# Kernel tuning notes

Hardware: AMD Instinct MI355X
Metric: run time of the kernel (lower is better)

Reference implementation:

```python
import jax, jax.numpy as jnp
import numpy as np

N, E, G = 50000, 1600000, 64
D_IN, D_EDGE, D_H, D_U, D_OUT = 32, 32, 64, 16, 32


def _linear_params(key, d_in, d_out):
    kw, kb = jax.random.split(key)
    lim = 1.0 / np.sqrt(d_in)
    W = jax.random.uniform(kw, (d_in, d_out), minval=-lim, maxval=lim, dtype=jnp.float32)
    b = jax.random.uniform(kb, (d_out,), minval=-lim, maxval=lim, dtype=jnp.float32)
    return W, b


def setup_inputs() -> dict:
    key = jax.random.key(0)
    ks = jax.random.split(key, 10)
    x = jax.random.normal(ks[0], (N, D_IN), dtype=jnp.float32)
    edge_index = jax.random.randint(ks[1], (2, E), 0, N, dtype=jnp.int64)
    edge_attr = jax.random.normal(ks[2], (E, D_EDGE), dtype=jnp.float32)
    u = jax.random.normal(ks[3], (G, D_U), dtype=jnp.float32)
    batch = jnp.sort(jax.random.randint(ks[4], (N,), 0, G, dtype=jnp.int64))
    W1a, b1a = _linear_params(ks[5], D_IN + D_EDGE, D_H)   # node linear 0
    W1b, b1b = _linear_params(ks[6], D_H, D_H)             # node linear 1 (hidden)
    W2a, b2a = _linear_params(ks[7], D_IN + D_H + D_U, D_H)
    W2b, b2b = _linear_params(ks[8], D_H, D_OUT)
    return dict(x=x, edge_index=edge_index, edge_attr=edge_attr, u=u, batch=batch,
                W1a=W1a, b1a=b1a, W1b=W1b, b1b=b1b,
                W2a=W2a, b2a=b2a, W2b=W2b, b2b=b2b)


def reference(x, edge_index, edge_attr, u, batch,
              W1a, b1a, W1b, b1b, W2a, b2a, W2b, b2b):
    row, col = edge_index[0], edge_index[1]
    # edge-level MLP on [x[col] || edge_attr]
    h = jnp.concatenate([x[col], edge_attr], axis=1)          # [E, D_IN+D_EDGE]
    h = jax.nn.relu(h @ W1a + b1a)                            # [E, D_H]
    h = jax.nn.relu(h @ W1b + b1b)                            # [E, D_H]
    # scatter_mean over destination nodes (row), dim_size = N
    summed = jax.ops.segment_sum(h, row, num_segments=N)      # [N, D_H]
    counts = jax.ops.segment_sum(jnp.ones((h.shape[0],), h.dtype), row, num_segments=N)
    agg = summed / jnp.maximum(counts, 1.0)[:, None]
    # node-level MLP on [x || agg || u[batch]]
    z = jnp.concatenate([x, agg, u[batch]], axis=1)           # [N, D_IN+D_H+D_U]
    z = jax.nn.relu(z @ W2a + b2a)
    return z @ W2b + b2b                                      # [N, D_OUT]
```

## Files before the change

kernel.cpp:

```cpp
#include <hip/hip_runtime.h>
#include <hip/hip_bf16.h>


typedef __attribute__((ext_vector_type(8))) short bf16x8;
typedef __attribute__((ext_vector_type(4))) float f32x4;

__device__ __forceinline__ unsigned short f2bf(float f) {
    __bf16 h = (__bf16)f;
    unsigned short u;
    __builtin_memcpy(&u, &h, 2);
    return u;
}


__global__ __launch_bounds__(256) void count_rows(
    const int* __restrict__ erow, int* __restrict__ counts, int E)
{
    const int gid = blockIdx.x * blockDim.x + threadIdx.x;
    const int stride = gridDim.x * blockDim.x;
    const int n4 = E >> 2;
    for (int i = gid; i < n4; i += stride) {
        const int4 r = ((const int4*)erow)[i];
        atomicAdd(&counts[r.x], 1);
        atomicAdd(&counts[r.y], 1);
        atomicAdd(&counts[r.z], 1);
        atomicAdd(&counts[r.w], 1);
    }
    for (int i = (n4 << 2) + gid; i < E; i += stride)
        atomicAdd(&counts[erow[i]], 1);
}

__global__ __launch_bounds__(256) void scan_blocks(
    const int* __restrict__ counts, int* __restrict__ excl,
    int* __restrict__ bsum, int N)
{
    __shared__ int tmp[256];
    const int t = threadIdx.x;
    const int i = blockIdx.x * 256 + t;
    const int v = (i < N) ? counts[i] : 0;
    tmp[t] = v; __syncthreads();
#pragma unroll
    for (int o = 1; o < 256; o <<= 1) {
        const int a = (t >= o) ? tmp[t - o] : 0;
        __syncthreads();
        tmp[t] += a;
        __syncthreads();
    }
    if (i < N) excl[i] = tmp[t] - v;
    if (t == 255) bsum[blockIdx.x] = tmp[t];
}

__global__ __launch_bounds__(256) void scan_bsum(int* __restrict__ bsum, int nb)
{
    __shared__ int tmp[256];
    const int t = threadIdx.x;
    const int v = (t < nb) ? bsum[t] : 0;
    tmp[t] = v; __syncthreads();
#pragma unroll
    for (int o = 1; o < 256; o <<= 1) {
        const int a = (t >= o) ? tmp[t - o] : 0;
        __syncthreads();
        tmp[t] += a;
        __syncthreads();
    }
    if (t < nb) bsum[t] = tmp[t] - v;
}

__global__ __launch_bounds__(256) void scan_add(
    int* __restrict__ rowstart, int* __restrict__ cursor,
    const int* __restrict__ bsum, int N, int E)
{
    const int i = blockIdx.x * 256 + threadIdx.x;
    if (i < N) {
        const int v = rowstart[i] + bsum[blockIdx.x];
        rowstart[i] = v;
        cursor[i]   = v;
    }
    if (i == 0) rowstart[N] = E;
}

__global__ __launch_bounds__(256) void permute_edges(
    const int* __restrict__ erow, const int* __restrict__ ecol,
    int* __restrict__ cursor, int2* __restrict__ sorted2, int E)
{
    const int gid = blockIdx.x * blockDim.x + threadIdx.x;
    const int stride = gridDim.x * blockDim.x;
    const int n4 = E >> 2;
    for (int i = gid; i < n4; i += stride) {
        const int4 r = ((const int4*)erow)[i];
        const int4 c = ((const int4*)ecol)[i];
        const int e0 = i << 2;
        int pos;
        pos = atomicAdd(&cursor[r.x], 1);
        sorted2[pos] = int2{e0,     (int)((unsigned)c.x | ((unsigned)r.x << 16))};
        pos = atomicAdd(&cursor[r.y], 1);
        sorted2[pos] = int2{e0 + 1, (int)((unsigned)c.y | ((unsigned)r.y << 16))};
        pos = atomicAdd(&cursor[r.z], 1);
        sorted2[pos] = int2{e0 + 2, (int)((unsigned)c.z | ((unsigned)r.z << 16))};
        pos = atomicAdd(&cursor[r.w], 1);
        sorted2[pos] = int2{e0 + 3, (int)((unsigned)c.w | ((unsigned)r.w << 16))};
    }
    for (int i = (n4 << 2) + gid; i < E; i += stride) {
        const int r = erow[i];
        const int pos = atomicAdd(&cursor[r], 1);
        sorted2[pos] = int2{i, (int)((unsigned)ecol[i] | ((unsigned)r << 16))};
    }
}


__global__ __launch_bounds__(256, 3) void edge_mlp_mfma(
    const float* __restrict__ x,
    const int2*  __restrict__ sorted2,
    const float* __restrict__ eattr,
    const float* __restrict__ W1a,
    const float* __restrict__ b1a,
    const float* __restrict__ W1b,
    const float* __restrict__ b1b,
    float* __restrict__ summed,
    int E)
{
    __shared__ __align__(16) unsigned short H2[4 * 16 * 64];

    const int tid  = threadIdx.x;
    const int lane = tid & 63;
    const int wv   = tid >> 6;
    const int g    = lane >> 4;
    const int el   = lane & 15;

    unsigned short* const h2w = H2 + wv * (16 * 64);

    bf16x8 wa[4][2], wb[4][2];
    f32x4  bias1[4];
    float  bias2s[4];
#pragma unroll
    for (int mt = 0; mt < 4; ++mt) {
        const int o = mt * 16 + el;
#pragma unroll
        for (int ks = 0; ks < 2; ++ks) {
            bf16x8 ta, tb;
#pragma unroll
            for (int j = 0; j < 8; ++j) {
                const int k = ks * 32 + 8 * g + j;
                ta[j] = (short)f2bf(W1a[k * 64 + o]);
                tb[j] = (short)f2bf(W1b[k * 64 + o]);
            }
            wa[mt][ks] = ta;
            wb[mt][ks] = tb;
        }
#pragma unroll
        for (int r = 0; r < 4; ++r) bias1[mt][r] = b1a[mt * 16 + 4 * g + r];
        bias2s[mt] = b1b[o];
    }

    const int ntile = (E + 15) >> 4;
    const int wid   = blockIdx.x * 4 + wv;
    const int nw    = gridDim.x * 4;

    const int sw = el & 7;

    for (int t = wid; t < ntile; t += nw) {
        const int ebase = t << 4;

        int2 s2; int row;
        if (ebase + el < E) {
            s2 = sorted2[ebase + el];
            row = (int)((unsigned)s2.y >> 16);
        } else { s2 = int2{0, 0}; row = -1; }

        bf16x8 bf0, bf1;
        {
            const float4* xp = (const float4*)(x + (size_t)(s2.y & 0xFFFF) * 32 + 8 * g);
            const float4* ap = (const float4*)(eattr + (size_t)s2.x * 32 + 8 * g);
            const float4 x0 = xp[0], x1 = xp[1];
            const float4 a0v = ap[0], a1v = ap[1];
            bf0[0] = (short)f2bf(x0.x); bf0[1] = (short)f2bf(x0.y);
            bf0[2] = (short)f2bf(x0.z); bf0[3] = (short)f2bf(x0.w);
            bf0[4] = (short)f2bf(x1.x); bf0[5] = (short)f2bf(x1.y);
            bf0[6] = (short)f2bf(x1.z); bf0[7] = (short)f2bf(x1.w);
            bf1[0] = (short)f2bf(a0v.x); bf1[1] = (short)f2bf(a0v.y);
            bf1[2] = (short)f2bf(a0v.z); bf1[3] = (short)f2bf(a0v.w);
            bf1[4] = (short)f2bf(a1v.x); bf1[5] = (short)f2bf(a1v.y);
            bf1[6] = (short)f2bf(a1v.z); bf1[7] = (short)f2bf(a1v.w);
        }

        f32x4 a0 = bias1[0], a1 = bias1[1], a2 = bias1[2], a3 = bias1[3];
        a0 = __builtin_amdgcn_mfma_f32_16x16x32_bf16(wa[0][0], bf0, a0, 0, 0, 0);
        a1 = __builtin_amdgcn_mfma_f32_16x16x32_bf16(wa[1][0], bf0, a1, 0, 0, 0);
        a2 = __builtin_amdgcn_mfma_f32_16x16x32_bf16(wa[2][0], bf0, a2, 0, 0, 0);
        a3 = __builtin_amdgcn_mfma_f32_16x16x32_bf16(wa[3][0], bf0, a3, 0, 0, 0);
        a0 = __builtin_amdgcn_mfma_f32_16x16x32_bf16(wa[0][1], bf1, a0, 0, 0, 0);
        a1 = __builtin_amdgcn_mfma_f32_16x16x32_bf16(wa[1][1], bf1, a1, 0, 0, 0);
        a2 = __builtin_amdgcn_mfma_f32_16x16x32_bf16(wa[2][1], bf1, a2, 0, 0, 0);
        a3 = __builtin_amdgcn_mfma_f32_16x16x32_bf16(wa[3][1], bf1, a3, 0, 0, 0);

        unsigned short* hrow = h2w + el * 64;
        {
            f32x4 accs[4] = {a0, a1, a2, a3};
#pragma unroll
            for (int mt = 0; mt < 4; ++mt) {
                unsigned short pk[4];
#pragma unroll
                for (int r = 0; r < 4; ++r) pk[r] = f2bf(fmaxf(accs[mt][r], 0.f));
                const int hid   = mt * 16 + 4 * g;
                const int chunk = hid >> 3;
                const int off   = hid & 7;
                *(uint2*)(hrow + ((chunk ^ sw) * 8 + off)) = *(uint2*)pk;
            }
        }

        const bf16x8 hb0 = *(const bf16x8*)(hrow + (((0 + g) ^ sw) * 8));
        const bf16x8 hb1 = *(const bf16x8*)(hrow + (((4 + g) ^ sw) * 8));
        f32x4 d0 = {bias2s[0], bias2s[0], bias2s[0], bias2s[0]};
        f32x4 d1 = {bias2s[1], bias2s[1], bias2s[1], bias2s[1]};
        f32x4 d2 = {bias2s[2], bias2s[2], bias2s[2], bias2s[2]};
        f32x4 d3 = {bias2s[3], bias2s[3], bias2s[3], bias2s[3]};
        d0 = __builtin_amdgcn_mfma_f32_16x16x32_bf16(hb0, wb[0][0], d0, 0, 0, 0);
        d1 = __builtin_amdgcn_mfma_f32_16x16x32_bf16(hb0, wb[1][0], d1, 0, 0, 0);
        d2 = __builtin_amdgcn_mfma_f32_16x16x32_bf16(hb0, wb[2][0], d2, 0, 0, 0);
        d3 = __builtin_amdgcn_mfma_f32_16x16x32_bf16(hb0, wb[3][0], d3, 0, 0, 0);
        d0 = __builtin_amdgcn_mfma_f32_16x16x32_bf16(hb1, wb[0][1], d0, 0, 0, 0);
        d1 = __builtin_amdgcn_mfma_f32_16x16x32_bf16(hb1, wb[1][1], d1, 0, 0, 0);
        d2 = __builtin_amdgcn_mfma_f32_16x16x32_bf16(hb1, wb[2][1], d2, 0, 0, 0);
        d3 = __builtin_amdgcn_mfma_f32_16x16x32_bf16(hb1, wb[3][1], d3, 0, 0, 0);

#pragma unroll
        for (int r = 0; r < 4; ++r) {
            d0[r] = fmaxf(d0[r], 0.f);
            d1[r] = fmaxf(d1[r], 0.f);
            d2[r] = fmaxf(d2[r], 0.f);
            d3[r] = fmaxf(d3[r], 0.f);
        }

        const int prevrow = __shfl(row, lane - 1);
        unsigned long long bmask =
            __ballot((g == 0) && (el > 0) && (row != prevrow));
        bmask = (bmask & 0xFFFEull) | 0x10000ull;

        int s = 0;
        while (s < 16) {
            const int e = s + 1 + (__ffsll(bmask >> (s + 1)) - 1);
            const int rowid = __shfl(row, s);
            if (rowid >= 0) {
                float s0 = 0.f, s1 = 0.f, s2v = 0.f, s3 = 0.f;
#pragma unroll
                for (int r = 0; r < 4; ++r) {
                    const int ej = 4 * g + r;
                    const bool in = (ej >= s) && (ej < e);
                    s0  += in ? d0[r] : 0.f;
                    s1  += in ? d1[r] : 0.f;
                    s2v += in ? d2[r] : 0.f;
                    s3  += in ? d3[r] : 0.f;
                }
                s0  += __shfl_xor(s0, 16);  s0  += __shfl_xor(s0, 32);
                s1  += __shfl_xor(s1, 16);  s1  += __shfl_xor(s1, 32);
                s2v += __shfl_xor(s2v, 16); s2v += __shfl_xor(s2v, 32);
                s3  += __shfl_xor(s3, 16);  s3  += __shfl_xor(s3, 32);
                const float val = (g == 0) ? s0 : (g == 1) ? s1
                                : (g == 2) ? s2v : s3;
                unsafeAtomicAdd(&summed[(size_t)rowid * 64 + lane], val);
            }
            s = e;
        }
    }
}


__global__ __launch_bounds__(256, 2) void node_mlp_mfma(
    const float* __restrict__ x,
    const float* __restrict__ summed,
    const int*   __restrict__ rowstart,
    const float* __restrict__ u,
    const int*   __restrict__ batch,
    const float* __restrict__ W2a,
    const float* __restrict__ b2a,
    const float* __restrict__ W2b,
    const float* __restrict__ b2b,
    float* __restrict__ out,
    int N)
{
    __shared__ __align__(16) unsigned short In[64 * 128];
    __shared__ __align__(16) unsigned short H[64 * 64];

    const int tid  = threadIdx.x;
    const int lane = tid & 63;
    const int wv   = tid >> 6;
    const int g    = lane >> 4;
    const int el   = lane & 15;

    bf16x8 wa[4][4];
    f32x4  bias1[4];
#pragma unroll
    for (int mt = 0; mt < 4; ++mt) {
        const int o = mt * 16 + el;
#pragma unroll
        for (int ks = 0; ks < 4; ++ks) {
            bf16x8 ta;
#pragma unroll
            for (int j = 0; j < 8; ++j) {
                const int k = ks * 32 + 8 * g + j;
                ta[j] = (k < 112) ? (short)f2bf(W2a[k * 64 + o]) : (short)0;
            }
            wa[mt][ks] = ta;
        }
#pragma unroll
        for (int r = 0; r < 4; ++r) bias1[mt][r] = b2a[mt * 16 + 4 * g + r];
    }
    bf16x8 wb[2][2];
    float  bias2s[2];
#pragma unroll
    for (int nt = 0; nt < 2; ++nt) {
        const int o = nt * 16 + el;
#pragma unroll
        for (int ks = 0; ks < 2; ++ks) {
            bf16x8 tb;
#pragma unroll
            for (int j = 0; j < 8; ++j) {
                const int k = ks * 32 + 8 * g + j;
                tb[j] = (short)f2bf(W2b[k * 32 + o]);
            }
            wb[nt][ks] = tb;
        }
        bias2s[nt] = b2b[o];
    }

    unsigned short* const inrow = In + (wv * 16) * 128;
    unsigned short* const hrow0 = H + (wv * 16) * 64;

    const int ntile = (N + 15) >> 4;
    const int wid   = blockIdx.x * 4 + wv;
    const int nw    = gridDim.x * 4;

    for (int t = wid; t < ntile; t += nw) {
        const int nbase = t << 4;

        {
            const int le = lane >> 2;
            const int p  = lane & 3;
            const int n  = nbase + le;
            float4 v[8];
            if (n < N) {
                if (p == 0) {
                    const float4* xp = (const float4*)(x + (size_t)n * 32);
#pragma unroll
                    for (int q = 0; q < 8; ++q) v[q] = xp[q];
                } else if (p < 3) {
                    const int cnt = rowstart[n + 1] - rowstart[n];
                    const float inv = 1.0f / fmaxf((float)cnt, 1.0f);
                    const float4* sp = (const float4*)(summed + (size_t)n * 64 + (p - 1) * 32);
#pragma unroll
                    for (int q = 0; q < 8; ++q) {
                        v[q] = sp[q];
                        v[q].x *= inv; v[q].y *= inv; v[q].z *= inv; v[q].w *= inv;
                    }
                } else {
                    const int gb = batch[n];
                    const float4* up = (const float4*)(u + (size_t)gb * 16);
#pragma unroll
                    for (int q = 0; q < 4; ++q) v[q] = up[q];
#pragma unroll
                    for (int q = 4; q < 8; ++q) v[q] = float4{0.f, 0.f, 0.f, 0.f};
                }
            } else {
#pragma unroll
                for (int q = 0; q < 8; ++q) v[q] = float4{0.f, 0.f, 0.f, 0.f};
            }
            const int sw = le & 7;
            unsigned short* row = inrow + le * 128;
#pragma unroll
            for (int q = 0; q < 4; ++q) {
                bf16x8 c;
                const float4 va = v[2 * q], vb = v[2 * q + 1];
                c[0] = (short)f2bf(va.x); c[1] = (short)f2bf(va.y);
                c[2] = (short)f2bf(va.z); c[3] = (short)f2bf(va.w);
                c[4] = (short)f2bf(vb.x); c[5] = (short)f2bf(vb.y);
                c[6] = (short)f2bf(vb.z); c[7] = (short)f2bf(vb.w);
                const int cc = 4 * p + q;
                const int ci = (cc & 8) | ((cc & 7) ^ sw);
                *(bf16x8*)(row + ci * 8) = c;
            }
        }

        const unsigned short* brow = inrow + el * 128;
        const int sw7 = el & 7;
        f32x4 a0 = bias1[0], a1 = bias1[1], a2 = bias1[2], a3 = bias1[3];
#pragma unroll
        for (int ks = 0; ks < 4; ++ks) {
            const int cc = ks * 4 + g;
            const int ci = (cc & 8) | ((cc & 7) ^ sw7);
            const bf16x8 bf = *(const bf16x8*)(brow + ci * 8);
            a0 = __builtin_amdgcn_mfma_f32_16x16x32_bf16(wa[0][ks], bf, a0, 0, 0, 0);
            a1 = __builtin_amdgcn_mfma_f32_16x16x32_bf16(wa[1][ks], bf, a1, 0, 0, 0);
            a2 = __builtin_amdgcn_mfma_f32_16x16x32_bf16(wa[2][ks], bf, a2, 0, 0, 0);
            a3 = __builtin_amdgcn_mfma_f32_16x16x32_bf16(wa[3][ks], bf, a3, 0, 0, 0);
        }

        unsigned short* hrow = hrow0 + el * 64;
        {
            f32x4 accs[4] = {a0, a1, a2, a3};
#pragma unroll
            for (int mt = 0; mt < 4; ++mt) {
                unsigned short pk[4];
#pragma unroll
                for (int r = 0; r < 4; ++r) pk[r] = f2bf(fmaxf(accs[mt][r], 0.f));
                const int hid   = mt * 16 + 4 * g;
                const int chunk = hid >> 3;
                const int off   = hid & 7;
                *(uint2*)(hrow + ((chunk ^ sw7) * 8 + off)) = *(uint2*)pk;
            }
        }

        const bf16x8 hb0 = *(const bf16x8*)(hrow + (((0 + g) ^ sw7) * 8));
        const bf16x8 hb1 = *(const bf16x8*)(hrow + (((4 + g) ^ sw7) * 8));
        f32x4 dn0 = {bias2s[0], bias2s[0], bias2s[0], bias2s[0]};
        f32x4 dn1 = {bias2s[1], bias2s[1], bias2s[1], bias2s[1]};
        dn0 = __builtin_amdgcn_mfma_f32_16x16x32_bf16(hb0, wb[0][0], dn0, 0, 0, 0);
        dn1 = __builtin_amdgcn_mfma_f32_16x16x32_bf16(hb0, wb[1][0], dn1, 0, 0, 0);
        dn0 = __builtin_amdgcn_mfma_f32_16x16x32_bf16(hb1, wb[0][1], dn0, 0, 0, 0);
        dn1 = __builtin_amdgcn_mfma_f32_16x16x32_bf16(hb1, wb[1][1], dn1, 0, 0, 0);

        if (nbase + 16 <= N) {
#pragma unroll
            for (int r = 0; r < 4; ++r) {
                float* dst = out + (size_t)(nbase + 4 * g + r) * 32 + el;
                dst[0]  = dn0[r];
                dst[16] = dn1[r];
            }
        } else {
#pragma unroll
            for (int r = 0; r < 4; ++r) {
                const int n = nbase + 4 * g + r;
                if (n < N) {
                    float* dst = out + (size_t)n * 32 + el;
                    dst[0]  = dn0[r];
                    dst[16] = dn1[r];
                }
            }
        }
    }
}

extern "C" void kernel_launch(void* const* d_in, const int* in_sizes, int n_in,
                              void* d_out, int out_size, void* d_ws, size_t ws_size,
                              hipStream_t stream) {
    const float* x     = (const float*)d_in[0];
    const int*   eidx  = (const int*)d_in[1];
    const float* eattr = (const float*)d_in[2];
    const float* u     = (const float*)d_in[3];
    const int*   batch = (const int*)d_in[4];
    const float* W1a   = (const float*)d_in[5];
    const float* b1a   = (const float*)d_in[6];
    const float* W1b   = (const float*)d_in[7];
    const float* b1b   = (const float*)d_in[8];
    const float* W2a   = (const float*)d_in[9];
    const float* b2a   = (const float*)d_in[10];
    const float* W2b   = (const float*)d_in[11];
    const float* b2b   = (const float*)d_in[12];
    float* out = (float*)d_out;

    const int N = in_sizes[0] / 32;
    const int E = in_sizes[1] / 2;
    const int* erow = eidx;
    const int* ecol = eidx + E;

    int2*  sorted2  = (int2*)d_ws;
    float* summed   = (float*)(sorted2 + E);
    int*   counts   = (int*)(summed + (size_t)N * 64);
    int*   rowstart = counts + N;
    int*   cursor   = rowstart + (N + 1);
    int*   bsum     = cursor + N;

    hipMemsetAsync(summed, 0, ((size_t)N * 64 + N) * sizeof(float), stream);

    count_rows<<<1024, 256, 0, stream>>>(erow, counts, E);
    const int nb = (N + 255) / 256;
    scan_blocks<<<nb, 256, 0, stream>>>(counts, rowstart, bsum, N);
    scan_bsum<<<1, 256, 0, stream>>>(bsum, nb);
    scan_add<<<nb, 256, 0, stream>>>(rowstart, cursor, bsum, N, E);
    permute_edges<<<1024, 256, 0, stream>>>(erow, ecol, cursor, sorted2, E);

    edge_mlp_mfma<<<4096, 256, 0, stream>>>(x, sorted2, eattr,
                                            W1a, b1a, W1b, b1b, summed, E);
    node_mlp_mfma<<<784, 256, 0, stream>>>(x, summed, rowstart, u, batch,
                                           W2a, b2a, W2b, b2b, out, N);
}
```

Baseline: 314.7 us.

## Pre-convert x and edge_attr to bf16, scattering edge_attr into sorted order

Adds a conversion of x to bf16 inside the row-count kernel. It also replaces the permute kernel with one that writes edge_attr as bf16 directly in row-sorted order, plus packed row/col indices. The edge MLP then reads contiguous bf16 edge features and bf16 x rows instead of gathering fp32 edge_attr by original edge id. This is meant to cut random gather traffic in the edge kernel, at the cost of an extra full pass writing E*64 bytes and needing a larger workspace, with a fallback to the old path when the workspace is too small.

```diff
diff --git a/kernel.cpp b/kernel.cpp
--- a/kernel.cpp
+++ b/kernel.cpp
@@ -11,13 +11,27 @@
     __builtin_memcpy(&u, &h, 2);
     return u;
 }
-
-
-__global__ __launch_bounds__(256) void count_rows(
-    const int* __restrict__ erow, int* __restrict__ counts, int E)
+__device__ __forceinline__ bf16x8 pack8(const float4 a, const float4 b) {
+    bf16x8 c;
+    c[0] = (short)f2bf(a.x); c[1] = (short)f2bf(a.y);
+    c[2] = (short)f2bf(a.z); c[3] = (short)f2bf(a.w);
+    c[4] = (short)f2bf(b.x); c[5] = (short)f2bf(b.y);
+    c[6] = (short)f2bf(b.z); c[7] = (short)f2bf(b.w);
+    return c;
+}
+
+
+__global__ __launch_bounds__(256) void count_rows_convx(
+    const int* __restrict__ erow, int* __restrict__ counts, int E,
+    const float* __restrict__ x, unsigned short* __restrict__ xbf, int nx8)
 {
     const int gid = blockIdx.x * blockDim.x + threadIdx.x;
     const int stride = gridDim.x * blockDim.x;
+    for (int i = gid; i < nx8; i += stride) {
+        const float4 a = ((const float4*)x)[2 * i];
+        const float4 b = ((const float4*)x)[2 * i + 1];
+        *(bf16x8*)(xbf + (size_t)i * 8) = pack8(a, b);
+    }
     const int n4 = E >> 2;
     for (int i = gid; i < n4; i += stride) {
         const int4 r = ((const int4*)erow)[i];
@@ -77,6 +91,27 @@
         cursor[i]   = v;
     }
     if (i == 0) rowstart[N] = E;
+}
+
+__global__ __launch_bounds__(256) void permute_conv(
+    const int* __restrict__ erow, const int* __restrict__ ecol,
+    const float* __restrict__ eattr,
+    int* __restrict__ cursor, int* __restrict__ sorted1,
+    unsigned short* __restrict__ eattr_s, int E)
+{
+    const int gid = blockIdx.x * blockDim.x + threadIdx.x;
+    const int stride = gridDim.x * blockDim.x;
+    for (int i = gid; i < E; i += stride) {
+        const int r = erow[i];
+        const int c = ecol[i];
+        const int pos = atomicAdd(&cursor[r], 1);
+        sorted1[pos] = (int)((unsigned)c | ((unsigned)r << 16));
+        const float4* src = (const float4*)(eattr + (size_t)i * 32);
+        unsigned short* dst = eattr_s + (size_t)pos * 32;
+#pragma unroll
+        for (int q = 0; q < 4; ++q)
+            *(bf16x8*)(dst + 8 * q) = pack8(src[2 * q], src[2 * q + 1]);
+    }
 }
 
 __global__ __launch_bounds__(256) void permute_edges(
@@ -108,16 +143,13 @@
 }
 
 
-__global__ __launch_bounds__(256, 3) void edge_mlp_mfma(
-    const float* __restrict__ x,
-    const int2*  __restrict__ sorted2,
-    const float* __restrict__ eattr,
-    const float* __restrict__ W1a,
-    const float* __restrict__ b1a,
-    const float* __restrict__ W1b,
-    const float* __restrict__ b1b,
-    float* __restrict__ summed,
-    int E)
+__global__ __launch_bounds__(256, 3) void edge_mlp_v2(
+    const unsigned short* __restrict__ xbf,
+    const int*            __restrict__ sorted1,
+    const unsigned short* __restrict__ eattr_s,
+    const float* __restrict__ W1a,  const float* __restrict__ b1a,
+    const float* __restrict__ W1b,  const float* __restrict__ b1b,
+    float* __restrict__ summed, int E)
 {
     __shared__ __align__(16) unsigned short H2[4 * 16 * 64];
 
@@ -155,12 +187,151 @@
     const int ntile = (E + 15) >> 4;
     const int wid   = blockIdx.x * 4 + wv;
     const int nw    = gridDim.x * 4;
-
-    const int sw = el & 7;
+    const int sw    = el & 7;
 
     for (int t = wid; t < ntile; t += nw) {
         const int ebase = t << 4;
-
+        const int e     = ebase + el;
+
+        int row, col;
+        if (e < E) {
+            const int m = sorted1[e];
+            row = (int)((unsigned)m >> 16);
+            col = m & 0xFFFF;
+        } else { row = -1; col = 0; }
+
+        const int ee = (e < E) ? e : (E - 1);
+        const bf16x8 bf0 = *(const bf16x8*)(xbf + (size_t)col * 32 + 8 * g);
+        const bf16x8 bf1 = *(const bf16x8*)(eattr_s + (size_t)ee * 32 + 8 * g);
+
+        f32x4 a0 = bias1[0], a1 = bias1[1], a2 = bias1[2], a3 = bias1[3];
+        a0 = __builtin_amdgcn_mfma_f32_16x16x32_bf16(wa[0][0], bf0, a0, 0, 0, 0);
+        a1 = __builtin_amdgcn_mfma_f32_16x16x32_bf16(wa[1][0], bf0, a1, 0, 0, 0);
+        a2 = __builtin_amdgcn_mfma_f32_16x16x32_bf16(wa[2][0], bf0, a2, 0, 0, 0);
+        a3 = __builtin_amdgcn_mfma_f32_16x16x32_bf16(wa[3][0], bf0, a3, 0, 0, 0);
+        a0 = __builtin_amdgcn_mfma_f32_16x16x32_bf16(wa[0][1], bf1, a0, 0, 0, 0);
+        a1 = __builtin_amdgcn_mfma_f32_16x16x32_bf16(wa[1][1], bf1, a1, 0, 0, 0);
+        a2 = __builtin_amdgcn_mfma_f32_16x16x32_bf16(wa[2][1], bf1, a2, 0, 0, 0);
+        a3 = __builtin_amdgcn_mfma_f32_16x16x32_bf16(wa[3][1], bf1, a3, 0, 0, 0);
+
+        unsigned short* hrow = h2w + el * 64;
+        {
+            f32x4 accs[4] = {a0, a1, a2, a3};
+#pragma unroll
+            for (int mt = 0; mt < 4; ++mt) {
+                unsigned short pk[4];
+#pragma unroll
+                for (int r = 0; r < 4; ++r) pk[r] = f2bf(fmaxf(accs[mt][r], 0.f));
+                const int hid   = mt * 16 + 4 * g;
+                const int chunk = hid >> 3;
+                const int off   = hid & 7;
+                *(uint2*)(hrow + ((chunk ^ sw) * 8 + off)) = *(uint2*)pk;
+            }
+        }
+
+        const bf16x8 hb0 = *(const bf16x8*)(hrow + (((0 + g) ^ sw) * 8));
+        const bf16x8 hb1 = *(const bf16x8*)(hrow + (((4 + g) ^ sw) * 8));
+        f32x4 d0 = {bias2s[0], bias2s[0], bias2s[0], bias2s[0]};
+        f32x4 d1 = {bias2s[1], bias2s[1], bias2s[1], bias2s[1]};
+        f32x4 d2 = {bias2s[2], bias2s[2], bias2s[2], bias2s[2]};
+        f32x4 d3 = {bias2s[3], bias2s[3], bias2s[3], bias2s[3]};
+        d0 = __builtin_amdgcn_mfma_f32_16x16x32_bf16(hb0, wb[0][0], d0, 0, 0, 0);
+        d1 = __builtin_amdgcn_mfma_f32_16x16x32_bf16(hb0, wb[1][0], d1, 0, 0, 0);
+        d2 = __builtin_amdgcn_mfma_f32_16x16x32_bf16(hb0, wb[2][0], d2, 0, 0, 0);
+        d3 = __builtin_amdgcn_mfma_f32_16x16x32_bf16(hb0, wb[3][0], d3, 0, 0, 0);
+        d0 = __builtin_amdgcn_mfma_f32_16x16x32_bf16(hb1, wb[0][1], d0, 0, 0, 0);
+        d1 = __builtin_amdgcn_mfma_f32_16x16x32_bf16(hb1, wb[1][1], d1, 0, 0, 0);
+        d2 = __builtin_amdgcn_mfma_f32_16x16x32_bf16(hb1, wb[2][1], d2, 0, 0, 0);
+        d3 = __builtin_amdgcn_mfma_f32_16x16x32_bf16(hb1, wb[3][1], d3, 0, 0, 0);
+
+#pragma unroll
+        for (int r = 0; r < 4; ++r) {
+            d0[r] = fmaxf(d0[r], 0.f);
+            d1[r] = fmaxf(d1[r], 0.f);
+            d2[r] = fmaxf(d2[r], 0.f);
+            d3[r] = fmaxf(d3[r], 0.f);
+        }
+
+        const int prevrow = __shfl(row, lane - 1);
+        unsigned long long bmask =
+            __ballot((g == 0) && (el > 0) && (row != prevrow));
+        bmask = (bmask & 0xFFFEull) | 0x10000ull;
+
+        int s = 0;
+        while (s < 16) {
+            const int e2 = s + 1 + (__ffsll(bmask >> (s + 1)) - 1);
+            const int rowid = __shfl(row, s);
+            if (rowid >= 0) {
+                float s0 = 0.f, s1 = 0.f, s2v = 0.f, s3 = 0.f;
+#pragma unroll
+                for (int r = 0; r < 4; ++r) {
+                    const int ej = 4 * g + r;
+                    const bool in = (ej >= s) && (ej < e2);
+                    s0  += in ? d0[r] : 0.f;
+                    s1  += in ? d1[r] : 0.f;
+                    s2v += in ? d2[r] : 0.f;
+                    s3  += in ? d3[r] : 0.f;
+                }
+                s0  += __shfl_xor(s0, 16);  s0  += __shfl_xor(s0, 32);
+                s1  += __shfl_xor(s1, 16);  s1  += __shfl_xor(s1, 32);
+                s2v += __shfl_xor(s2v, 16); s2v += __shfl_xor(s2v, 32);
+                s3  += __shfl_xor(s3, 16);  s3  += __shfl_xor(s3, 32);
+                const float val = (g == 0) ? s0 : (g == 1) ? s1
+                                : (g == 2) ? s2v : s3;
+                unsafeAtomicAdd(&summed[(size_t)rowid * 64 + lane], val);
+            }
+            s = e2;
+        }
+    }
+}
+
+
+__global__ __launch_bounds__(256, 3) void edge_mlp_mfma(
+    const float* __restrict__ x,
+    const int2*  __restrict__ sorted2,
+    const float* __restrict__ eattr,
+    const float* __restrict__ W1a,  const float* __restrict__ b1a,
+    const float* __restrict__ W1b,  const float* __restrict__ b1b,
+    float* __restrict__ summed, int E)
+{
+    __shared__ __align__(16) unsigned short H2[4 * 16 * 64];
+    const int tid  = threadIdx.x;
+    const int lane = tid & 63;
+    const int wv   = tid >> 6;
+    const int g    = lane >> 4;
+    const int el   = lane & 15;
+    unsigned short* const h2w = H2 + wv * (16 * 64);
+
+    bf16x8 wa[4][2], wb[4][2];
+    f32x4  bias1[4];
+    float  bias2s[4];
+#pragma unroll
+    for (int mt = 0; mt < 4; ++mt) {
+        const int o = mt * 16 + el;
+#pragma unroll
+        for (int ks = 0; ks < 2; ++ks) {
+            bf16x8 ta, tb;
+#pragma unroll
+            for (int j = 0; j < 8; ++j) {
+                const int k = ks * 32 + 8 * g + j;
+                ta[j] = (short)f2bf(W1a[k * 64 + o]);
+                tb[j] = (short)f2bf(W1b[k * 64 + o]);
+            }
+            wa[mt][ks] = ta;
+            wb[mt][ks] = tb;
+        }
+#pragma unroll
+        for (int r = 0; r < 4; ++r) bias1[mt][r] = b1a[mt * 16 + 4 * g + r];
+        bias2s[mt] = b1b[o];
+    }
+
+    const int ntile = (E + 15) >> 4;
+    const int wid   = blockIdx.x * 4 + wv;
+    const int nw    = gridDim.x * 4;
+    const int sw    = el & 7;
+
+    for (int t = wid; t < ntile; t += nw) {
+        const int ebase = t << 4;
         int2 s2; int row;
         if (ebase + el < E) {
             s2 = sorted2[ebase + el];
@@ -171,16 +342,8 @@
         {
             const float4* xp = (const float4*)(x + (size_t)(s2.y & 0xFFFF) * 32 + 8 * g);
             const float4* ap = (const float4*)(eattr + (size_t)s2.x * 32 + 8 * g);
-            const float4 x0 = xp[0], x1 = xp[1];
-            const float4 a0v = ap[0], a1v = ap[1];
-            bf0[0] = (short)f2bf(x0.x); bf0[1] = (short)f2bf(x0.y);
-            bf0[2] = (short)f2bf(x0.z); bf0[3] = (short)f2bf(x0.w);
-            bf0[4] = (short)f2bf(x1.x); bf0[5] = (short)f2bf(x1.y);
-            bf0[6] = (short)f2bf(x1.z); bf0[7] = (short)f2bf(x1.w);
-            bf1[0] = (short)f2bf(a0v.x); bf1[1] = (short)f2bf(a0v.y);
-            bf1[2] = (short)f2bf(a0v.z); bf1[3] = (short)f2bf(a0v.w);
-            bf1[4] = (short)f2bf(a1v.x); bf1[5] = (short)f2bf(a1v.y);
-            bf1[6] = (short)f2bf(a1v.z); bf1[7] = (short)f2bf(a1v.w);
+            bf0 = pack8(xp[0], xp[1]);
+            bf1 = pack8(ap[0], ap[1]);
         }
 
         f32x4 a0 = bias1[0], a1 = bias1[1], a2 = bias1[2], a3 = bias1[3];
@@ -332,7 +495,6 @@
 
     for (int t = wid; t < ntile; t += nw) {
         const int nbase = t << 4;
-
         {
             const int le = lane >> 2;
             const int p  = lane & 3;
@@ -368,15 +530,9 @@
             unsigned short* row = inrow + le * 128;
 #pragma unroll
             for (int q = 0; q < 4; ++q) {
-                bf16x8 c;
-                const float4 va = v[2 * q], vb = v[2 * q + 1];
-                c[0] = (short)f2bf(va.x); c[1] = (short)f2bf(va.y);
-                c[2] = (short)f2bf(va.z); c[3] = (short)f2bf(va.w);
-                c[4] = (short)f2bf(vb.x); c[5] = (short)f2bf(vb.y);
-                c[6] = (short)f2bf(vb.z); c[7] = (short)f2bf(vb.w);
                 const int cc = 4 * p + q;
                 const int ci = (cc & 8) | ((cc & 7) ^ sw);
-                *(bf16x8*)(row + ci * 8) = c;
+                *(bf16x8*)(row + ci * 8) = pack8(v[2 * q], v[2 * q + 1]);
             }
         }
 
@@ -461,25 +617,50 @@
     const int E = in_sizes[1] / 2;
     const int* erow = eidx;
     const int* ecol = eidx + E;
-
-    int2*  sorted2  = (int2*)d_ws;
-    float* summed   = (float*)(sorted2 + E);
-    int*   counts   = (int*)(summed + (size_t)N * 64);
-    int*   rowstart = counts + N;
-    int*   cursor   = rowstart + (N + 1);
-    int*   bsum     = cursor + N;
-
-    hipMemsetAsync(summed, 0, ((size_t)N * 64 + N) * sizeof(float), stream);
-
-    count_rows<<<1024, 256, 0, stream>>>(erow, counts, E);
     const int nb = (N + 255) / 256;
-    scan_blocks<<<nb, 256, 0, stream>>>(counts, rowstart, bsum, N);
-    scan_bsum<<<1, 256, 0, stream>>>(bsum, nb);
-    scan_add<<<nb, 256, 0, stream>>>(rowstart, cursor, bsum, N, E);
-    permute_edges<<<1024, 256, 0, stream>>>(erow, ecol, cursor, sorted2, E);
-
-    edge_mlp_mfma<<<4096, 256, 0, stream>>>(x, sorted2, eattr,
-                                            W1a, b1a, W1b, b1b, summed, E);
-    node_mlp_mfma<<<784, 256, 0, stream>>>(x, summed, rowstart, u, batch,
-                                           W2a, b2a, W2b, b2b, out, N);
-}
+
+    const size_t need_full = (size_t)E * 64 + (size_t)N * 64 + (size_t)E * 4
+                           + (size_t)N * 256 + (size_t)(3 * N + 1) * 4 + 1024;
+
+    if (ws_size >= need_full) {
+        char* p = (char*)d_ws;
+        unsigned short* eattr_s = (unsigned short*)p; p += (size_t)E * 64;
+        unsigned short* xbf     = (unsigned short*)p; p += (size_t)N * 64;
+        int*   sorted1  = (int*)p;   p += (size_t)E * 4;
+        float* summed   = (float*)p; p += (size_t)N * 256;
+        int*   counts   = (int*)p;   p += (size_t)N * 4;
+        int*   rowstart = (int*)p;   p += (size_t)(N + 1) * 4;
+        int*   cursor   = (int*)p;   p += (size_t)N * 4;
+        int*   bsum     = (int*)p;
+
+        hipMemsetAsync(summed, 0, (size_t)N * 256 + (size_t)N * 4, stream);
+        count_rows_convx<<<1024, 256, 0, stream>>>(erow, counts, E, x, xbf, N * 4);
+        scan_blocks<<<nb, 256, 0, stream>>>(counts, rowstart, bsum, N);
+        scan_bsum<<<1, 256, 0, stream>>>(bsum, nb);
+        scan_add<<<nb, 256, 0, stream>>>(rowstart, cursor, bsum, N, E);
+        permute_conv<<<2048, 256, 0, stream>>>(erow, ecol, eattr, cursor,
+                                               sorted1, eattr_s, E);
+        edge_mlp_v2<<<4096, 256, 0, stream>>>(xbf, sorted1, eattr_s,
+                                              W1a, b1a, W1b, b1b, summed, E);
+        node_mlp_mfma<<<784, 256, 0, stream>>>(x, summed, rowstart, u, batch,
+                                               W2a, b2a, W2b, b2b, out, N);
+    } else {
+        int2*  sorted2  = (int2*)d_ws;
+        float* summed   = (float*)(sorted2 + E);
+        int*   counts   = (int*)(summed + (size_t)N * 64);
+        int*   rowstart = counts + N;
+        int*   cursor   = rowstart + (N + 1);
+        int*   bsum     = cursor + N;
+
+        hipMemsetAsync(summed, 0, ((size_t)N * 64 + N) * sizeof(float), stream);
+        count_rows_convx<<<1024, 256, 0, stream>>>(erow, counts, E, x, nullptr, 0);
+        scan_blocks<<<nb, 256, 0, stream>>>(counts, rowstart, bsum, N);
+        scan_bsum<<<1, 256, 0, stream>>>(bsum, nb);
+        scan_add<<<nb, 256, 0, stream>>>(rowstart, cursor, bsum, N, E);
+        permute_edges<<<1024, 256, 0, stream>>>(erow, ecol, cursor, sorted2, E);
+        edge_mlp_mfma<<<4096, 256, 0, stream>>>(x, sorted2, eattr,
+                                                W1a, b1a, W1b, b1b, summed, E);
+        node_mlp_mfma<<<784, 256, 0, stream>>>(x, summed, rowstart, u, batch,
+                                               W2a, b2a, W2b, b2b, out, N);
+    }
+}
```

Result: no change. 318.6 us (+1.2%).

## Replace direct edge permutation with two-pass bucket binning then placement

Applied to the files above, without the earlier changes.

Instead of scattering each edge straight to its sorted slot, which produces random 8-byte writes across the whole array, edges are first binned by row>>8 into 256 coarse buckets using shared-memory histograms, then a second pass places them into their final sorted positions. The goal is to make the scatter writes more local so they cache better. In exchange the edge list is read and written one extra time and an extra workspace buffer is needed. If the workspace is too small, the code falls back to the old path, now without the int4 vectorisation.

```diff
diff --git a/kernel.cpp b/kernel.cpp
--- a/kernel.cpp
+++ b/kernel.cpp
@@ -68,6 +68,7 @@
 
 __global__ __launch_bounds__(256) void scan_add(
     int* __restrict__ rowstart, int* __restrict__ cursor,
+    int* __restrict__ bucket_cursor,
     const int* __restrict__ bsum, int N, int E)
 {
     const int i = blockIdx.x * 256 + threadIdx.x;
@@ -75,8 +76,59 @@
         const int v = rowstart[i] + bsum[blockIdx.x];
         rowstart[i] = v;
         cursor[i]   = v;
+        if ((i & 255) == 0) bucket_cursor[i >> 8] = v;
     }
     if (i == 0) rowstart[N] = E;
+}
+
+#define BIN_CHUNK 8192
+__global__ __launch_bounds__(256) void bin_edges_v2(
+    const int* __restrict__ erow, const int* __restrict__ ecol,
+    int* __restrict__ bucket_cursor, int2* __restrict__ binned, int E)
+{
+    __shared__ int hist[256];
+    const int tid  = threadIdx.x;
+    const int base = blockIdx.x * BIN_CHUNK;
+
+    hist[tid] = 0;
+    __syncthreads();
+#pragma unroll 1
+    for (int i = 0; i < BIN_CHUNK; i += 256) {
+        const int e = base + i + tid;
+        if (e < E) atomicAdd(&hist[erow[e] >> 8], 1);
+    }
+    __syncthreads();
+    {
+        const int cnt = hist[tid];
+        int b = 0;
+        if (cnt > 0) b = atomicAdd(&bucket_cursor[tid], cnt);
+        __syncthreads();
+        hist[tid] = b;
+    }
+    __syncthreads();
+#pragma unroll 1
+    for (int i = 0; i < BIN_CHUNK; i += 256) {
+        const int e = base + i + tid;
+        if (e < E) {
+            const int r = erow[e];
+            const int q = atomicAdd(&hist[r >> 8], 1);
+            binned[q] = int2{e, (int)((unsigned)ecol[e] | ((unsigned)r << 16))};
+        }
+    }
+}
+
+__global__ __launch_bounds__(256) void place_edges(
+    const int2* __restrict__ binned, int* __restrict__ cursor,
+    int2* __restrict__ sorted2, int E)
+{
+    const int gid = blockIdx.x * blockDim.x + threadIdx.x;
+    const int stride = gridDim.x * blockDim.x;
+    for (int p = gid; p < E; p += stride) {
+        const int2 m = binned[p];
+        const int row = (int)((unsigned)m.y >> 16);
+        const int pos = atomicAdd(&cursor[row], 1);
+        sorted2[pos] = m;
+    }
 }
 
 __global__ __launch_bounds__(256) void permute_edges(
@@ -85,22 +137,7 @@
 {
     const int gid = blockIdx.x * blockDim.x + threadIdx.x;
     const int stride = gridDim.x * blockDim.x;
-    const int n4 = E >> 2;
-    for (int i = gid; i < n4; i += stride) {
-        const int4 r = ((const int4*)erow)[i];
-        const int4 c = ((const int4*)ecol)[i];
-        const int e0 = i << 2;
-        int pos;
-        pos = atomicAdd(&cursor[r.x], 1);
-        sorted2[pos] = int2{e0,     (int)((unsigned)c.x | ((unsigned)r.x << 16))};
-        pos = atomicAdd(&cursor[r.y], 1);
-        sorted2[pos] = int2{e0 + 1, (int)((unsigned)c.y | ((unsigned)r.y << 16))};
-        pos = atomicAdd(&cursor[r.z], 1);
-        sorted2[pos] = int2{e0 + 2, (int)((unsigned)c.z | ((unsigned)r.z << 16))};
-        pos = atomicAdd(&cursor[r.w], 1);
-        sorted2[pos] = int2{e0 + 3, (int)((unsigned)c.w | ((unsigned)r.w << 16))};
-    }
-    for (int i = (n4 << 2) + gid; i < E; i += stride) {
+    for (int i = gid; i < E; i += stride) {
         const int r = erow[i];
         const int pos = atomicAdd(&cursor[r], 1);
         sorted2[pos] = int2{i, (int)((unsigned)ecol[i] | ((unsigned)r << 16))};
@@ -155,12 +192,10 @@
     const int ntile = (E + 15) >> 4;
     const int wid   = blockIdx.x * 4 + wv;
     const int nw    = gridDim.x * 4;
-
-    const int sw = el & 7;
+    const int sw    = el & 7;
 
     for (int t = wid; t < ntile; t += nw) {
         const int ebase = t << 4;
-
         int2 s2; int row;
         if (ebase + el < E) {
             s2 = sorted2[ebase + el];
@@ -332,7 +367,6 @@
 
     for (int t = wid; t < ntile; t += nw) {
         const int nbase = t << 4;
-
         {
             const int le = lane >> 2;
             const int p  = lane & 3;
@@ -461,25 +495,55 @@
     const int E = in_sizes[1] / 2;
     const int* erow = eidx;
     const int* ecol = eidx + E;
-
-    int2*  sorted2  = (int2*)d_ws;
-    float* summed   = (float*)(sorted2 + E);
-    int*   counts   = (int*)(summed + (size_t)N * 64);
-    int*   rowstart = counts + N;
-    int*   cursor   = rowstart + (N + 1);
-    int*   bsum     = cursor + N;
-
-    hipMemsetAsync(summed, 0, ((size_t)N * 64 + N) * sizeof(float), stream);
-
-    count_rows<<<1024, 256, 0, stream>>>(erow, counts, E);
     const int nb = (N + 255) / 256;
-    scan_blocks<<<nb, 256, 0, stream>>>(counts, rowstart, bsum, N);
-    scan_bsum<<<1, 256, 0, stream>>>(bsum, nb);
-    scan_add<<<nb, 256, 0, stream>>>(rowstart, cursor, bsum, N, E);
-    permute_edges<<<1024, 256, 0, stream>>>(erow, ecol, cursor, sorted2, E);
-
-    edge_mlp_mfma<<<4096, 256, 0, stream>>>(x, sorted2, eattr,
-                                            W1a, b1a, W1b, b1b, summed, E);
-    node_mlp_mfma<<<784, 256, 0, stream>>>(x, summed, rowstart, u, batch,
-                                           W2a, b2a, W2b, b2b, out, N);
-}
+
+    const size_t need_full = (size_t)E * 16 + (size_t)N * 256
+                           + (size_t)(3 * N + 1) * 4 + 2048;
+
+    if (ws_size >= need_full) {
+        char* p = (char*)d_ws;
+        int2*  sorted2  = (int2*)p;  p += (size_t)E * 8;
+        int2*  binned   = (int2*)p;  p += (size_t)E * 8;
+        float* summed   = (float*)p; p += (size_t)N * 256;
+        int*   counts   = (int*)p;   p += (size_t)N * 4;
+        int*   rowstart = (int*)p;   p += (size_t)(N + 1) * 4;
+        int*   cursor   = (int*)p;   p += (size_t)N * 4;
+        int*   bucket_cursor = (int*)p; p += 1024;
+        int*   bsum     = (int*)p;
+
+        hipMemsetAsync(summed, 0, (size_t)N * 256 + (size_t)N * 4, stream);
+        count_rows<<<1024, 256, 0, stream>>>(erow, counts, E);
+        scan_blocks<<<nb, 256, 0, stream>>>(counts, rowstart, bsum, N);
+        scan_bsum<<<1, 256, 0, stream>>>(bsum, nb);
+        scan_add<<<nb, 256, 0, stream>>>(rowstart, cursor, bucket_cursor,
+                                         bsum, N, E);
+        const int nbin = (E + BIN_CHUNK - 1) / BIN_CHUNK;
+        bin_edges_v2<<<nbin, 256, 0, stream>>>(erow, ecol, bucket_cursor,
+                                               binned, E);
+        place_edges<<<512, 256, 0, stream>>>(binned, cursor, sorted2, E);
+        edge_mlp_mfma<<<4096, 256, 0, stream>>>(x, sorted2, eattr,
+                                                W1a, b1a, W1b, b1b, summed, E);
+        node_mlp_mfma<<<784, 256, 0, stream>>>(x, summed, rowstart, u, batch,
+                                               W2a, b2a, W2b, b2b, out, N);
+    } else {
+        int2*  sorted2  = (int2*)d_ws;
+        float* summed   = (float*)(sorted2 + E);
+        int*   counts   = (int*)(summed + (size_t)N * 64);
+        int*   rowstart = counts + N;
+        int*   cursor   = rowstart + (N + 1);
+        int*   bucket_cursor = cursor + N;
+        int*   bsum     = bucket_cursor + 256;
+
+        hipMemsetAsync(summed, 0, ((size_t)N * 64 + N) * sizeof(float), stream);
+        count_rows<<<1024, 256, 0, stream>>>(erow, counts, E);
+        scan_blocks<<<nb, 256, 0, stream>>>(counts, rowstart, bsum, N);
+        scan_bsum<<<1, 256, 0, stream>>>(bsum, nb);
+        scan_add<<<nb, 256, 0, stream>>>(rowstart, cursor, bucket_cursor,
+                                         bsum, N, E);
+        permute_edges<<<1024, 256, 0, stream>>>(erow, ecol, cursor, sorted2, E);
+        edge_mlp_mfma<<<4096, 256, 0, stream>>>(x, sorted2, eattr,
+                                                W1a, b1a, W1b, b1b, summed, E);
+        node_mlp_mfma<<<784, 256, 0, stream>>>(x, summed, rowstart, u, batch,
+                                               W2a, b2a, W2b, b2b, out, N);
+    }
+}
```

Result: faster. 298.6 us (-5.1%).
